# Optimization experiments

Hardware: AMD Instinct MI355X
Metric: run time of the kernel (lower is better)

The kernel has to match this reference:

```python
import jax, jax.numpy as jnp
import numpy as np

B, D_IN, NF = 8192, 64, 128
D1 = 1 + D_IN              # 65  : first linear input (bias col + x)
O1 = 1 + NF                # 129 : o width after first layer
IN2 = O1 + NF * NF         # 16513 : polylayer-1 input width
O2 = O1 + NF               # 257
IN3 = O2 + NF * NF         # 16641 : polylayer-2 input width
FC_IN = 1 + 3 * NF + 3 * NF  # 769 : cat(o, og) width


def setup_inputs() -> dict:
    key = jax.random.key(0)
    ks = jax.random.split(key, 16)
    w = lambda k, shape: jax.random.normal(k, shape, jnp.float32) * 0.02
    return {
        "x": jax.random.normal(ks[0], (B, D_IN), jnp.float32),
        "bias0": jnp.asarray(1.0, jnp.float32),
        "Wf1": w(ks[1], (D1, NF)), "bf1": w(ks[2], (NF,)),
        "Wg1": w(ks[3], (D1, NF)), "bg1": w(ks[4], (NF,)),
        "Wf2": w(ks[5], (IN2, NF)), "bf2": w(ks[6], (NF,)),
        "Wg2": w(ks[7], (IN2, NF)), "bg2": w(ks[8], (NF,)),
        "Wf3": w(ks[9], (IN3, NF)), "bf3": w(ks[10], (NF,)),
        "Wg3": w(ks[11], (IN3, NF)), "bg3": w(ks[12], (NF,)),
        "Wfc": w(ks[13], (FC_IN, 1)), "bfc": w(ks[14], (1,)),
    }


def reference(x, bias0, Wf1, bf1, Wg1, bg1, Wf2, bf2, Wg2, bg2,
              Wf3, bf3, Wg3, bg3, Wfc, bfc):
    Bn = x.shape[0]
    o = jnp.ones((Bn, 1), x.dtype) * bias0          # bias column
    z = jnp.concatenate([o, x], axis=1)              # [B, 1+D_in]
    og = z @ Wg1 + bg1                               # vanishing branch
    ot = z @ Wf1 + bf1                               # nonvanishing branch
    o1 = ot                                          # degree-1 features, kept fixed
    o = jnp.concatenate([o, ot], axis=1)
    for Wf, bf, Wg, bg in ((Wf2, bf2, Wg2, bg2), (Wf3, bf3, Wg3, bg3)):
        # batched outer product o1_i ot_i^T, row-major flatten -> [B, nf1*nf_t]
        outer = (o1[:, :, None] * ot[:, None, :]).reshape(Bn, -1)
        xx = jnp.concatenate([o, outer], axis=1)
        xf = xx @ Wf + bf
        xg = xx @ Wg + bg
        ot = xf
        o = jnp.concatenate([o, xf], axis=1)
        og = jnp.concatenate([og, xg], axis=1)
    return jnp.concatenate([o, og], axis=1) @ Wfc + bfc
```

## Files before the change

kernel.cpp:

```cpp
#include <hip/hip_runtime.h>

typedef _Float16 f16;
typedef _Float16 f16x8 __attribute__((ext_vector_type(8)));
typedef float f32x4 __attribute__((ext_vector_type(4)));

static constexpr size_t PART_STRIDE = (size_t)8192 * 256;

static constexpr size_t OFF_W2   = 0;
static constexpr size_t SZ_W2    = (size_t)516 * 8192 * 2;
static constexpr size_t OFF_W3   = OFF_W2 + SZ_W2;
static constexpr size_t SZ_W3    = (size_t)520 * 8192 * 2;
static constexpr size_t OFF_OT1  = OFF_W3 + SZ_W3;
static constexpr size_t OFF_XF2  = OFF_OT1 + (size_t)8192 * 128 * 2;
static constexpr size_t OFF_C2   = OFF_XF2 + (size_t)8192 * 128 * 2;
static constexpr size_t OFF_C3   = OFF_C2 + 1024;
static constexpr size_t OFF_ACC  = OFF_C3 + 1024;
static constexpr size_t OFF_PART = OFF_ACC + 32768;

template<int LAYER>
__global__ __launch_bounds__(256)
void prep_w(const float* __restrict__ Wf, const float* __restrict__ Wg,
            f16* __restrict__ Wswz)
{
    const int t = blockIdx.x * 256 + threadIdx.x;
    const int s = t >> 10, rem = t & 1023;
    const int nt = rem >> 6, l = rem & 63;
    const int n = nt * 16 + (l & 15);
    const int klb = (l >> 4) * 8;
    f16x8 o;
#pragma unroll
    for (int e = 0; e < 8; ++e) {
        const int kl = klb + e;
        int row;
        if (LAYER == 2) {
            if (s < 4) row = 1 + s * 32 + kl;
            else { const int u = s - 4; row = 129 + (u & 127) * 128 + (u >> 7) * 32 + kl; }
        } else {
            if (s < 8) row = 1 + s * 32 + kl;
            else { const int u = s - 8; row = 257 + (u & 127) * 128 + (u >> 7) * 32 + kl; }
        }
        const float v = (n < 128) ? Wf[(size_t)row * 128 + n]
                                  : Wg[(size_t)row * 128 + (n - 128)];
        o[e] = (f16)v;
    }
    *(f16x8*)(Wswz + (size_t)t * 8) = o;
}

__global__ __launch_bounds__(256)
void prep_small(const float* __restrict__ bias0,
                const float* __restrict__ Wf2, const float* __restrict__ bf2,
                const float* __restrict__ Wg2, const float* __restrict__ bg2,
                const float* __restrict__ Wf3, const float* __restrict__ bf3,
                const float* __restrict__ Wg3, const float* __restrict__ bg3,
                float* __restrict__ c2, float* __restrict__ c3)
{
    const int n = threadIdx.x;
    const float b0 = bias0[0];
    if (n < 128) { c2[n] = bf2[n] + b0 * Wf2[n]; c3[n] = bf3[n] + b0 * Wf3[n]; }
    else { const int m = n - 128; c2[n] = bg2[m] + b0 * Wg2[m]; c3[n] = bg3[m] + b0 * Wg3[m]; }
}

__global__ __launch_bounds__(256)
void layer1_poly(const float* __restrict__ x, const float* __restrict__ bias0,
                 const float* __restrict__ Wf1, const float* __restrict__ bf1,
                 const float* __restrict__ Wg1, const float* __restrict__ bg1,
                 const float* __restrict__ Wfc, const float* __restrict__ bfc,
                 f16* __restrict__ ot1f16, float* __restrict__ outacc)
{
    const int half = threadIdx.x >> 7;
    const int n = threadIdx.x & 127;
    const int r = blockIdx.x * 2 + half;
    const float b0 = bias0[0];
    float sf = b0 * Wf1[n] + bf1[n];
    float sg = b0 * Wg1[n] + bg1[n];
    const float* xr = x + (size_t)r * 64;
#pragma unroll 8
    for (int k = 0; k < 64; ++k) {
        const float xv = xr[k];
        sf = fmaf(xv, Wf1[(k + 1) * 128 + n], sf);
        sg = fmaf(xv, Wg1[(k + 1) * 128 + n], sg);
    }
    ot1f16[(size_t)r * 128 + n] = (f16)sf;
    float p = sf * Wfc[1 + n] + sg * Wfc[385 + n];
#pragma unroll
    for (int off = 32; off; off >>= 1) p += __shfl_down(p, off);
    __shared__ float wp[4];
    if ((threadIdx.x & 63) == 0) wp[threadIdx.x >> 6] = p;
    __syncthreads();
    if ((threadIdx.x & 127) == 0)
        outacc[r] = bfc[0] + b0 * Wfc[0] + wp[half * 2] + wp[half * 2 + 1];
}


#define STAGE(S_W, BUF) do {                                                        \
    const f16* _src = wsrc0 + (size_t)(S_W) * 8192;                                 \
    __builtin_amdgcn_global_load_lds(                                               \
        (const __attribute__((address_space(1))) unsigned int*)_src,                \
        (__attribute__((address_space(3))) unsigned int*)&wbuf[BUF][tid * 8],       \
        16, 0, 0);                                                                  \
} while (0)

#define GBODY(O1CUR, O1NXT, I8)                                                     \
{                                                                                   \
    _Pragma("unroll")                                                               \
    for (int e = 0; e < 8; ++e) {                                                   \
        const int cc = (I8) * 8 + e;                                                \
        if (e < 7) { STAGE(out_base + cc + 1, (CLIN + e + 1) & 1); }                \
        else if ((I8) < 15) { STAGE(out_base + cc + 1, (CLIN + e + 1) & 1); }       \
        if (e == 0) {                                                               \
            _Pragma("unroll")                                                       \
            for (int mi = 0; mi < 8; ++mi)                                          \
                O1NXT[mi] = *(const f16x8*)(ot1_row + mi * 2048 + ((I8) + 1) * 8);  \
        }                                                                           \
        f16x8 afr[8];                                                               \
        _Pragma("unroll")                                                           \
        for (int mi = 0; mi < 8; ++mi)                                              \
            afr[mi] = featreg[mi] * O1CUR[mi][e];                                   \
        const f16* wb = &wbuf[(CLIN + e) & 1][0];                                   \
        _Pragma("unroll")                                                           \
        for (int ni = 0; ni < 2; ++ni) {                                            \
            const f16x8 bfr = *(const f16x8*)(wb + ((wc * 2 + ni) * 64 + lane) * 8);\
            _Pragma("unroll")                                                       \
            for (int mi = 0; mi < 8; ++mi)                                          \
                acc[mi][ni] = __builtin_amdgcn_mfma_f32_16x16x32_f16(               \
                    afr[mi], bfr, acc[mi][ni], 0, 0, 0);                            \
        }                                                                           \
        __syncthreads();                                                            \
    }                                                                               \
}

template<int LAYER>
__global__ __launch_bounds__(256, 2)
void gemm_poly(const f16* __restrict__ Wswz, const f16* featg,
               const f16* ot1g, float* __restrict__ partials)
{
    __shared__ f16 wbuf[2][2048];

    constexpr int NLIN = (LAYER == 2) ? 4 : 8;
    constexpr int CLIN = (LAYER == 2) ? 1 : 2;

    const int bid = blockIdx.x;
    const int rb = bid >> 4;
    const int sp = (bid >> 2) & 3;
    const int nb = bid & 3;
    const int r0 = rb * 256;
    const int tid = threadIdx.x;
    const int wid = tid >> 6, lane = tid & 63;
    const int wr = wid >> 1, wc = wid & 1;
    const int lhi = lane >> 4, llo = lane & 15;

    const f16* wsrc0 = Wswz + nb * 2048 + tid * 8;
    const f16* ot1_row  = ot1g  + (size_t)(r0 + wr * 128 + llo) * 128;
    const f16* feat_row = featg + (size_t)(r0 + wr * 128 + llo) * 128;

    f32x4 acc[8][2] = {};
    const int out_base = NLIN + sp * 128;

    STAGE(CLIN * sp, 0);
    f16x8 featreg[8], o1A[8], o1B[8];
#pragma unroll
    for (int mi = 0; mi < 8; ++mi) {
        featreg[mi] = *(const f16x8*)(feat_row + mi * 2048 + sp * 32 + lhi * 8);
        o1A[mi]     = *(const f16x8*)(ot1_row + mi * 2048);
    }
    __syncthreads();

#pragma unroll
    for (int c = 0; c < CLIN; ++c) {
        const int s = CLIN * sp + c;
        STAGE((c + 1 < CLIN) ? (s + 1) : out_base, (c + 1) & 1);
        f16x8 afr[8];
        const int col = s * 32 + lhi * 8;
#pragma unroll
        for (int mi = 0; mi < 8; ++mi) {
            if (LAYER == 2) afr[mi] = *(const f16x8*)(ot1_row + mi * 2048 + col);
            else afr[mi] = (col < 128) ? *(const f16x8*)(ot1_row + mi * 2048 + col)
                                       : *(const f16x8*)(feat_row + mi * 2048 + (col - 128));
        }
        const f16* wb = &wbuf[c & 1][0];
#pragma unroll
        for (int ni = 0; ni < 2; ++ni) {
            const f16x8 bfr = *(const f16x8*)(wb + ((wc * 2 + ni) * 64 + lane) * 8);
#pragma unroll
            for (int mi = 0; mi < 8; ++mi)
                acc[mi][ni] = __builtin_amdgcn_mfma_f32_16x16x32_f16(afr[mi], bfr, acc[mi][ni], 0, 0, 0);
        }
        __syncthreads();
    }

    for (int i8 = 0; i8 < 16; i8 += 2) {
        GBODY(o1A, o1B, i8);
        GBODY(o1B, o1A, i8 + 1);
    }

    float* pout = partials + (size_t)sp * PART_STRIDE
                + (size_t)(r0 + wr * 128) * 256 + nb * 64 + wc * 32 + llo;
#pragma unroll
    for (int mi = 0; mi < 8; ++mi)
#pragma unroll
        for (int ni = 0; ni < 2; ++ni)
#pragma unroll
            for (int q = 0; q < 4; ++q)
                pout[(size_t)(mi * 16 + lhi * 4 + q) * 256 + ni * 16] = acc[mi][ni][q];
}

#undef GBODY
#undef STAGE

template<int LAYER>
__global__ __launch_bounds__(256)
void reduce_poly(const float* __restrict__ partials, const float* __restrict__ cvec,
                 const float* __restrict__ Wfc, f16* __restrict__ xf_out,
                 float* __restrict__ outacc, float* __restrict__ outp)
{
    const int r = blockIdx.x;
    const int n = threadIdx.x;
    const size_t idx = (size_t)r * 256 + n;
    float v = partials[idx] + partials[idx + PART_STRIDE]
            + partials[idx + 2 * PART_STRIDE] + partials[idx + 3 * PART_STRIDE];
    v += cvec[n];
    if (LAYER == 2 && n < 128)
        xf_out[(size_t)r * 128 + n] = (f16)v;
    const int wseg = (LAYER == 2) ? (n < 128 ? 129 + n : 513 + (n - 128))
                                  : (n < 128 ? 257 + n : 641 + (n - 128));
    float p = v * Wfc[wseg];
#pragma unroll
    for (int off = 32; off; off >>= 1) p += __shfl_down(p, off);
    __shared__ float wp[4];
    if ((threadIdx.x & 63) == 0) wp[threadIdx.x >> 6] = p;
    __syncthreads();
    if (threadIdx.x == 0) {
        const float tot = wp[0] + wp[1] + wp[2] + wp[3];
        if (LAYER == 2) outacc[r] += tot;
        else            outp[r] = outacc[r] + tot;
    }
}

extern "C" void kernel_launch(void* const* d_in, const int* in_sizes, int n_in,
                              void* d_out, int out_size, void* d_ws, size_t ws_size,
                              hipStream_t stream)
{
    (void)in_sizes; (void)n_in; (void)out_size; (void)ws_size;
    const float* x     = (const float*)d_in[0];
    const float* bias0 = (const float*)d_in[1];
    const float* Wf1   = (const float*)d_in[2];
    const float* bf1   = (const float*)d_in[3];
    const float* Wg1   = (const float*)d_in[4];
    const float* bg1   = (const float*)d_in[5];
    const float* Wf2   = (const float*)d_in[6];
    const float* bf2   = (const float*)d_in[7];
    const float* Wg2   = (const float*)d_in[8];
    const float* bg2   = (const float*)d_in[9];
    const float* Wf3   = (const float*)d_in[10];
    const float* bf3   = (const float*)d_in[11];
    const float* Wg3   = (const float*)d_in[12];
    const float* bg3   = (const float*)d_in[13];
    const float* Wfc   = (const float*)d_in[14];
    const float* bfc   = (const float*)d_in[15];
    float* out = (float*)d_out;

    char* ws = (char*)d_ws;
    f16*   W2s    = (f16*)(ws + OFF_W2);
    f16*   W3s    = (f16*)(ws + OFF_W3);
    f16*   ot1f16 = (f16*)(ws + OFF_OT1);
    f16*   xf2f16 = (f16*)(ws + OFF_XF2);
    float* c2     = (float*)(ws + OFF_C2);
    float* c3     = (float*)(ws + OFF_C3);
    float* outacc = (float*)(ws + OFF_ACC);
    float* parts  = (float*)(ws + OFF_PART);

    prep_w<2><<<2064, 256, 0, stream>>>(Wf2, Wg2, W2s);
    prep_w<3><<<2080, 256, 0, stream>>>(Wf3, Wg3, W3s);
    prep_small<<<1, 256, 0, stream>>>(bias0, Wf2, bf2, Wg2, bg2, Wf3, bf3, Wg3, bg3, c2, c3);
    layer1_poly<<<4096, 256, 0, stream>>>(x, bias0, Wf1, bf1, Wg1, bg1, Wfc, bfc, ot1f16, outacc);
    gemm_poly<2><<<512, 256, 0, stream>>>(W2s, ot1f16, ot1f16, parts);
    reduce_poly<2><<<8192, 256, 0, stream>>>(parts, c2, Wfc, xf2f16, outacc, out);
    gemm_poly<3><<<512, 256, 0, stream>>>(W3s, xf2f16, ot1f16, parts);
    reduce_poly<3><<<8192, 256, 0, stream>>>(parts, c3, Wfc, nullptr, outacc, out);
}
```

Before: 312.6 us.

## Load B fragments straight from global into registers, drop LDS staging and barriers

The poly GEMM no longer stages weight tiles through double-buffered LDS with a barrier per k-step. Each wave now loads its own B fragment directly from global memory into registers, using a two-deep register prefetch. The N tile per block is halved (one 16-column fragment per wave), the grid doubles to 1024 blocks, and launch bounds allow 4 blocks per CU. This removes synchronisation and LDS traffic and raises occupancy. In exchange, each wave issues global loads with less latency hiding, the A fragment products are recomputed for half as many columns, and more blocks redundantly load the same A rows.

```diff
diff --git a/kernel.cpp b/kernel.cpp
--- a/kernel.cpp
+++ b/kernel.cpp
@@ -92,120 +92,92 @@
 }
 
 
-#define STAGE(S_W, BUF) do {                                                        \
-    const f16* _src = wsrc0 + (size_t)(S_W) * 8192;                                 \
-    __builtin_amdgcn_global_load_lds(                                               \
-        (const __attribute__((address_space(1))) unsigned int*)_src,                \
-        (__attribute__((address_space(3))) unsigned int*)&wbuf[BUF][tid * 8],       \
-        16, 0, 0);                                                                  \
-} while (0)
-
-#define GBODY(O1CUR, O1NXT, I8)                                                     \
+#define OBODY(O1CUR, O1NXT, I8)                                                     \
 {                                                                                   \
     _Pragma("unroll")                                                               \
     for (int e = 0; e < 8; ++e) {                                                   \
         const int cc = (I8) * 8 + e;                                                \
-        if (e < 7) { STAGE(out_base + cc + 1, (CLIN + e + 1) & 1); }                \
-        else if ((I8) < 15) { STAGE(out_base + cc + 1, (CLIN + e + 1) & 1); }       \
+        f16x8 bC = {};                                                              \
+        if (cc + 2 < 128)                                                           \
+            bC = *(const f16x8*)(wB + (size_t)(out_base + cc + 2) * 8192);          \
         if (e == 0) {                                                               \
             _Pragma("unroll")                                                       \
             for (int mi = 0; mi < 8; ++mi)                                          \
                 O1NXT[mi] = *(const f16x8*)(ot1_row + mi * 2048 + ((I8) + 1) * 8);  \
         }                                                                           \
-        f16x8 afr[8];                                                               \
         _Pragma("unroll")                                                           \
-        for (int mi = 0; mi < 8; ++mi)                                              \
-            afr[mi] = featreg[mi] * O1CUR[mi][e];                                   \
-        const f16* wb = &wbuf[(CLIN + e) & 1][0];                                   \
-        _Pragma("unroll")                                                           \
-        for (int ni = 0; ni < 2; ++ni) {                                            \
-            const f16x8 bfr = *(const f16x8*)(wb + ((wc * 2 + ni) * 64 + lane) * 8);\
-            _Pragma("unroll")                                                       \
-            for (int mi = 0; mi < 8; ++mi)                                          \
-                acc[mi][ni] = __builtin_amdgcn_mfma_f32_16x16x32_f16(               \
-                    afr[mi], bfr, acc[mi][ni], 0, 0, 0);                            \
+        for (int mi = 0; mi < 8; ++mi) {                                            \
+            const f16x8 a = featreg[mi] * O1CUR[mi][e];                             \
+            acc[mi] = __builtin_amdgcn_mfma_f32_16x16x32_f16(a, bA, acc[mi], 0, 0, 0);\
         }                                                                           \
-        __syncthreads();                                                            \
+        bA = bB; bB = bC;                                                           \
     }                                                                               \
 }
 
 template<int LAYER>
-__global__ __launch_bounds__(256, 2)
+__global__ __launch_bounds__(256, 4)
 void gemm_poly(const f16* __restrict__ Wswz, const f16* featg,
                const f16* ot1g, float* __restrict__ partials)
 {
-    __shared__ f16 wbuf[2][2048];
-
     constexpr int NLIN = (LAYER == 2) ? 4 : 8;
     constexpr int CLIN = (LAYER == 2) ? 1 : 2;
 
     const int bid = blockIdx.x;
-    const int rb = bid >> 4;
-    const int sp = (bid >> 2) & 3;
-    const int nb = bid & 3;
+    const int rb = bid >> 5;
+    const int sp = (bid >> 3) & 3;
+    const int nb = bid & 7;
     const int r0 = rb * 256;
     const int tid = threadIdx.x;
     const int wid = tid >> 6, lane = tid & 63;
     const int wr = wid >> 1, wc = wid & 1;
     const int lhi = lane >> 4, llo = lane & 15;
 
-    const f16* wsrc0 = Wswz + nb * 2048 + tid * 8;
+    const f16* wB = Wswz + nb * 1024 + wc * 512 + lane * 8;
     const f16* ot1_row  = ot1g  + (size_t)(r0 + wr * 128 + llo) * 128;
     const f16* feat_row = featg + (size_t)(r0 + wr * 128 + llo) * 128;
 
-    f32x4 acc[8][2] = {};
+    f32x4 acc[8] = {};
     const int out_base = NLIN + sp * 128;
 
-    STAGE(CLIN * sp, 0);
     f16x8 featreg[8], o1A[8], o1B[8];
 #pragma unroll
     for (int mi = 0; mi < 8; ++mi) {
         featreg[mi] = *(const f16x8*)(feat_row + mi * 2048 + sp * 32 + lhi * 8);
         o1A[mi]     = *(const f16x8*)(ot1_row + mi * 2048);
     }
-    __syncthreads();
+    f16x8 bA = *(const f16x8*)(wB + (size_t)(out_base + 0) * 8192);
+    f16x8 bB = *(const f16x8*)(wB + (size_t)(out_base + 1) * 8192);
 
 #pragma unroll
     for (int c = 0; c < CLIN; ++c) {
         const int s = CLIN * sp + c;
-        STAGE((c + 1 < CLIN) ? (s + 1) : out_base, (c + 1) & 1);
-        f16x8 afr[8];
+        const f16x8 b = *(const f16x8*)(wB + (size_t)s * 8192);
         const int col = s * 32 + lhi * 8;
 #pragma unroll
         for (int mi = 0; mi < 8; ++mi) {
-            if (LAYER == 2) afr[mi] = *(const f16x8*)(ot1_row + mi * 2048 + col);
-            else afr[mi] = (col < 128) ? *(const f16x8*)(ot1_row + mi * 2048 + col)
-                                       : *(const f16x8*)(feat_row + mi * 2048 + (col - 128));
+            f16x8 a;
+            if (LAYER == 2) a = *(const f16x8*)(ot1_row + mi * 2048 + col);
+            else a = (col < 128) ? *(const f16x8*)(ot1_row + mi * 2048 + col)
+                                 : *(const f16x8*)(feat_row + mi * 2048 + (col - 128));
+            acc[mi] = __builtin_amdgcn_mfma_f32_16x16x32_f16(a, b, acc[mi], 0, 0, 0);
         }
-        const f16* wb = &wbuf[c & 1][0];
-#pragma unroll
-        for (int ni = 0; ni < 2; ++ni) {
-            const f16x8 bfr = *(const f16x8*)(wb + ((wc * 2 + ni) * 64 + lane) * 8);
-#pragma unroll
-            for (int mi = 0; mi < 8; ++mi)
-                acc[mi][ni] = __builtin_amdgcn_mfma_f32_16x16x32_f16(afr[mi], bfr, acc[mi][ni], 0, 0, 0);
-        }
-        __syncthreads();
     }
 
     for (int i8 = 0; i8 < 16; i8 += 2) {
-        GBODY(o1A, o1B, i8);
-        GBODY(o1B, o1A, i8 + 1);
+        OBODY(o1A, o1B, i8);
+        OBODY(o1B, o1A, i8 + 1);
     }
 
     float* pout = partials + (size_t)sp * PART_STRIDE
-                + (size_t)(r0 + wr * 128) * 256 + nb * 64 + wc * 32 + llo;
+                + (size_t)(r0 + wr * 128) * 256 + nb * 32 + wc * 16 + llo;
 #pragma unroll
     for (int mi = 0; mi < 8; ++mi)
 #pragma unroll
-        for (int ni = 0; ni < 2; ++ni)
-#pragma unroll
-            for (int q = 0; q < 4; ++q)
-                pout[(size_t)(mi * 16 + lhi * 4 + q) * 256 + ni * 16] = acc[mi][ni][q];
-}
-
-#undef GBODY
-#undef STAGE
+        for (int q = 0; q < 4; ++q)
+            pout[(size_t)(mi * 16 + lhi * 4 + q) * 256] = acc[mi][q];
+}
+
+#undef OBODY
 
 template<int LAYER>
 __global__ __launch_bounds__(256)
@@ -273,8 +245,8 @@
     prep_w<3><<<2080, 256, 0, stream>>>(Wf3, Wg3, W3s);
     prep_small<<<1, 256, 0, stream>>>(bias0, Wf2, bf2, Wg2, bg2, Wf3, bf3, Wg3, bg3, c2, c3);
     layer1_poly<<<4096, 256, 0, stream>>>(x, bias0, Wf1, bf1, Wg1, bg1, Wfc, bfc, ot1f16, outacc);
-    gemm_poly<2><<<512, 256, 0, stream>>>(W2s, ot1f16, ot1f16, parts);
+    gemm_poly<2><<<1024, 256, 0, stream>>>(W2s, ot1f16, ot1f16, parts);
     reduce_poly<2><<<8192, 256, 0, stream>>>(parts, c2, Wfc, xf2f16, outacc, out);
-    gemm_poly<3><<<512, 256, 0, stream>>>(W3s, xf2f16, ot1f16, parts);
+    gemm_poly<3><<<1024, 256, 0, stream>>>(W3s, xf2f16, ot1f16, parts);
     reduce_poly<3><<<8192, 256, 0, stream>>>(parts, c3, Wfc, nullptr, outacc, out);
 }
```

Measured after the change: 368.1 us. 1.18x slower.

## Fuse prep kernels into one launch and triple-buffer weight staging in GEMM

Applied to the files above, without the earlier changes.

Merges the two weight-swizzle kernels, the bias-constant kernel and the layer-1 kernel into a single launch that dispatches work by block index, removing three launch gaps. In the GEMM, the double-buffered LDS weight staging with a full __syncthreads per step becomes a 3-deep ring. Each step uses an explicit vmcnt wait plus s_barrier, so the async global-to-LDS load of step s+2 overlaps the MFMAs of step s. This adds LDS use and depends on the hand-written waitcnt counts being correct. It also issues a redundant tail stage load.

```diff
diff --git a/kernel.cpp b/kernel.cpp
--- a/kernel.cpp
+++ b/kernel.cpp
@@ -18,11 +18,10 @@
 static constexpr size_t OFF_PART = OFF_ACC + 32768;
 
 template<int LAYER>
-__global__ __launch_bounds__(256)
-void prep_w(const float* __restrict__ Wf, const float* __restrict__ Wg,
-            f16* __restrict__ Wswz)
-{
-    const int t = blockIdx.x * 256 + threadIdx.x;
+__device__ __forceinline__
+void prep_w_body(int t, const float* __restrict__ Wf, const float* __restrict__ Wg,
+                 f16* __restrict__ Wswz)
+{
     const int s = t >> 10, rem = t & 1023;
     const int nt = rem >> 6, l = rem & 63;
     const int n = nt * 16 + (l & 15);
@@ -47,48 +46,52 @@
 }
 
 __global__ __launch_bounds__(256)
-void prep_small(const float* __restrict__ bias0,
+void prep_fused(const float* __restrict__ x, const float* __restrict__ bias0,
+                const float* __restrict__ Wf1, const float* __restrict__ bf1,
+                const float* __restrict__ Wg1, const float* __restrict__ bg1,
                 const float* __restrict__ Wf2, const float* __restrict__ bf2,
                 const float* __restrict__ Wg2, const float* __restrict__ bg2,
                 const float* __restrict__ Wf3, const float* __restrict__ bf3,
                 const float* __restrict__ Wg3, const float* __restrict__ bg3,
-                float* __restrict__ c2, float* __restrict__ c3)
-{
-    const int n = threadIdx.x;
-    const float b0 = bias0[0];
-    if (n < 128) { c2[n] = bf2[n] + b0 * Wf2[n]; c3[n] = bf3[n] + b0 * Wf3[n]; }
-    else { const int m = n - 128; c2[n] = bg2[m] + b0 * Wg2[m]; c3[n] = bg3[m] + b0 * Wg3[m]; }
-}
-
-__global__ __launch_bounds__(256)
-void layer1_poly(const float* __restrict__ x, const float* __restrict__ bias0,
-                 const float* __restrict__ Wf1, const float* __restrict__ bf1,
-                 const float* __restrict__ Wg1, const float* __restrict__ bg1,
-                 const float* __restrict__ Wfc, const float* __restrict__ bfc,
-                 f16* __restrict__ ot1f16, float* __restrict__ outacc)
-{
-    const int half = threadIdx.x >> 7;
-    const int n = threadIdx.x & 127;
-    const int r = blockIdx.x * 2 + half;
-    const float b0 = bias0[0];
-    float sf = b0 * Wf1[n] + bf1[n];
-    float sg = b0 * Wg1[n] + bg1[n];
-    const float* xr = x + (size_t)r * 64;
+                const float* __restrict__ Wfc, const float* __restrict__ bfc,
+                f16* __restrict__ W2s, f16* __restrict__ W3s,
+                float* __restrict__ c2, float* __restrict__ c3,
+                f16* __restrict__ ot1f16, float* __restrict__ outacc)
+{
+    const int bid = blockIdx.x;
+    __shared__ float wp[4];
+    if (bid < 2064) {
+        prep_w_body<2>(bid * 256 + threadIdx.x, Wf2, Wg2, W2s);
+    } else if (bid < 4144) {
+        prep_w_body<3>((bid - 2064) * 256 + threadIdx.x, Wf3, Wg3, W3s);
+    } else if (bid == 4144) {
+        const int n = threadIdx.x;
+        const float b0 = bias0[0];
+        if (n < 128) { c2[n] = bf2[n] + b0 * Wf2[n]; c3[n] = bf3[n] + b0 * Wf3[n]; }
+        else { const int m = n - 128; c2[n] = bg2[m] + b0 * Wg2[m]; c3[n] = bg3[m] + b0 * Wg3[m]; }
+    } else {
+        const int half = threadIdx.x >> 7;
+        const int n = threadIdx.x & 127;
+        const int r = (bid - 4145) * 2 + half;
+        const float b0 = bias0[0];
+        float sf = b0 * Wf1[n] + bf1[n];
+        float sg = b0 * Wg1[n] + bg1[n];
+        const float* xr = x + (size_t)r * 64;
 #pragma unroll 8
-    for (int k = 0; k < 64; ++k) {
-        const float xv = xr[k];
-        sf = fmaf(xv, Wf1[(k + 1) * 128 + n], sf);
-        sg = fmaf(xv, Wg1[(k + 1) * 128 + n], sg);
-    }
-    ot1f16[(size_t)r * 128 + n] = (f16)sf;
-    float p = sf * Wfc[1 + n] + sg * Wfc[385 + n];
-#pragma unroll
-    for (int off = 32; off; off >>= 1) p += __shfl_down(p, off);
-    __shared__ float wp[4];
-    if ((threadIdx.x & 63) == 0) wp[threadIdx.x >> 6] = p;
-    __syncthreads();
-    if ((threadIdx.x & 127) == 0)
-        outacc[r] = bfc[0] + b0 * Wfc[0] + wp[half * 2] + wp[half * 2 + 1];
+        for (int k = 0; k < 64; ++k) {
+            const float xv = xr[k];
+            sf = fmaf(xv, Wf1[(k + 1) * 128 + n], sf);
+            sg = fmaf(xv, Wg1[(k + 1) * 128 + n], sg);
+        }
+        ot1f16[(size_t)r * 128 + n] = (f16)sf;
+        float p = sf * Wfc[1 + n] + sg * Wfc[385 + n];
+#pragma unroll
+        for (int off = 32; off; off >>= 1) p += __shfl_down(p, off);
+        if ((threadIdx.x & 63) == 0) wp[threadIdx.x >> 6] = p;
+        __syncthreads();
+        if ((threadIdx.x & 127) == 0)
+            outacc[r] = bfc[0] + b0 * Wfc[0] + wp[half * 2] + wp[half * 2 + 1];
+    }
 }
 
 
@@ -96,45 +99,55 @@
     const f16* _src = wsrc0 + (size_t)(S_W) * 8192;                                 \
     __builtin_amdgcn_global_load_lds(                                               \
         (const __attribute__((address_space(1))) unsigned int*)_src,                \
-        (__attribute__((address_space(3))) unsigned int*)&wbuf[BUF][tid * 8],       \
+        (__attribute__((address_space(3))) unsigned int*)&wring[BUF][tid * 8],      \
         16, 0, 0);                                                                  \
 } while (0)
 
-#define GBODY(O1CUR, O1NXT, I8)                                                     \
+#define WAITVX(N) asm volatile("s_waitcnt vmcnt(" #N ") lgkmcnt(0)" ::: "memory")
+#define WAITV(N) WAITVX(N)
+
+#define RSTEP(O1CUR, O1NXT, I8, E, WN, LN)                                          \
 {                                                                                   \
-    _Pragma("unroll")                                                               \
-    for (int e = 0; e < 8; ++e) {                                                   \
-        const int cc = (I8) * 8 + e;                                                \
-        if (e < 7) { STAGE(out_base + cc + 1, (CLIN + e + 1) & 1); }                \
-        else if ((I8) < 15) { STAGE(out_base + cc + 1, (CLIN + e + 1) & 1); }       \
-        if (e == 0) {                                                               \
-            _Pragma("unroll")                                                       \
-            for (int mi = 0; mi < 8; ++mi)                                          \
-                O1NXT[mi] = *(const f16x8*)(ot1_row + mi * 2048 + ((I8) + 1) * 8);  \
-        }                                                                           \
-        f16x8 afr[8];                                                               \
+    const int s_ = (I8) * 8 + (E);                                                  \
+    WAITV(WN);                                                                      \
+    __builtin_amdgcn_s_barrier();                                                   \
+    __builtin_amdgcn_sched_barrier(0);                                              \
+    {                                                                               \
+        const int sn_ = (s_ + 2 < 128) ? s_ + 2 : 127;           \
+        STAGE(out_base + sn_, (s_ + 2) % 3);                                        \
+    }                                                                               \
+    if ((LN) && (E) == 0) {                                                         \
         _Pragma("unroll")                                                           \
         for (int mi = 0; mi < 8; ++mi)                                              \
-            afr[mi] = featreg[mi] * O1CUR[mi][e];                                   \
-        const f16* wb = &wbuf[(CLIN + e) & 1][0];                                   \
-        _Pragma("unroll")                                                           \
-        for (int ni = 0; ni < 2; ++ni) {                                            \
-            const f16x8 bfr = *(const f16x8*)(wb + ((wc * 2 + ni) * 64 + lane) * 8);\
-            _Pragma("unroll")                                                       \
-            for (int mi = 0; mi < 8; ++mi)                                          \
-                acc[mi][ni] = __builtin_amdgcn_mfma_f32_16x16x32_f16(               \
-                    afr[mi], bfr, acc[mi][ni], 0, 0, 0);                            \
-        }                                                                           \
-        __syncthreads();                                                            \
+            O1NXT[mi] = *(const f16x8*)(ot1_row + mi * 2048 + ((I8) + 1) * 8);      \
     }                                                                               \
-}
+    const f16* wb_ = &wring[s_ % 3][0];                                             \
+    const f16x8 b0_ = *(const f16x8*)(wb_ + (wc * 128 + lane) * 8);                 \
+    const f16x8 b1_ = *(const f16x8*)(wb_ + (wc * 128 + 64 + lane) * 8);            \
+    _Pragma("unroll")                                                               \
+    for (int mi = 0; mi < 8; ++mi) {                                                \
+        const f16x8 a_ = featreg[mi] * O1CUR[mi][E];                                \
+        acc[mi][0] = __builtin_amdgcn_mfma_f32_16x16x32_f16(a_, b0_, acc[mi][0], 0, 0, 0); \
+        acc[mi][1] = __builtin_amdgcn_mfma_f32_16x16x32_f16(a_, b1_, acc[mi][1], 0, 0, 0); \
+    }                                                                               \
+}
+
+#define RBODY(O1CUR, O1NXT, I8, W1, LN)     \
+    RSTEP(O1CUR, O1NXT, I8, 0, 1, LN)       \
+    RSTEP(O1CUR, O1NXT, I8, 1, W1, LN)      \
+    RSTEP(O1CUR, O1NXT, I8, 2, 1, LN)       \
+    RSTEP(O1CUR, O1NXT, I8, 3, 1, LN)       \
+    RSTEP(O1CUR, O1NXT, I8, 4, 1, LN)       \
+    RSTEP(O1CUR, O1NXT, I8, 5, 1, LN)       \
+    RSTEP(O1CUR, O1NXT, I8, 6, 1, LN)       \
+    RSTEP(O1CUR, O1NXT, I8, 7, 1, LN)
 
 template<int LAYER>
 __global__ __launch_bounds__(256, 2)
 void gemm_poly(const f16* __restrict__ Wswz, const f16* featg,
                const f16* ot1g, float* __restrict__ partials)
 {
-    __shared__ f16 wbuf[2][2048];
+    __shared__ f16 wring[3][2048];
 
     constexpr int NLIN = (LAYER == 2) ? 4 : 8;
     constexpr int CLIN = (LAYER == 2) ? 1 : 2;
@@ -156,42 +169,44 @@
     f32x4 acc[8][2] = {};
     const int out_base = NLIN + sp * 128;
 
-    STAGE(CLIN * sp, 0);
     f16x8 featreg[8], o1A[8], o1B[8];
 #pragma unroll
     for (int mi = 0; mi < 8; ++mi) {
         featreg[mi] = *(const f16x8*)(feat_row + mi * 2048 + sp * 32 + lhi * 8);
         o1A[mi]     = *(const f16x8*)(ot1_row + mi * 2048);
     }
+
+    STAGE(CLIN * sp, 0);
     __syncthreads();
-
 #pragma unroll
     for (int c = 0; c < CLIN; ++c) {
+        if (c + 1 < CLIN) STAGE(CLIN * sp + c + 1, 1);
         const int s = CLIN * sp + c;
-        STAGE((c + 1 < CLIN) ? (s + 1) : out_base, (c + 1) & 1);
-        f16x8 afr[8];
         const int col = s * 32 + lhi * 8;
+        const f16* wb = &wring[c][0];
+        const f16x8 b0 = *(const f16x8*)(wb + (wc * 128 + lane) * 8);
+        const f16x8 b1 = *(const f16x8*)(wb + (wc * 128 + 64 + lane) * 8);
 #pragma unroll
         for (int mi = 0; mi < 8; ++mi) {
-            if (LAYER == 2) afr[mi] = *(const f16x8*)(ot1_row + mi * 2048 + col);
-            else afr[mi] = (col < 128) ? *(const f16x8*)(ot1_row + mi * 2048 + col)
-                                       : *(const f16x8*)(feat_row + mi * 2048 + (col - 128));
-        }
-        const f16* wb = &wbuf[c & 1][0];
-#pragma unroll
-        for (int ni = 0; ni < 2; ++ni) {
-            const f16x8 bfr = *(const f16x8*)(wb + ((wc * 2 + ni) * 64 + lane) * 8);
-#pragma unroll
-            for (int mi = 0; mi < 8; ++mi)
-                acc[mi][ni] = __builtin_amdgcn_mfma_f32_16x16x32_f16(afr[mi], bfr, acc[mi][ni], 0, 0, 0);
+            f16x8 a;
+            if (LAYER == 2) a = *(const f16x8*)(ot1_row + mi * 2048 + col);
+            else a = (col < 128) ? *(const f16x8*)(ot1_row + mi * 2048 + col)
+                                 : *(const f16x8*)(feat_row + mi * 2048 + (col - 128));
+            acc[mi][0] = __builtin_amdgcn_mfma_f32_16x16x32_f16(a, b0, acc[mi][0], 0, 0, 0);
+            acc[mi][1] = __builtin_amdgcn_mfma_f32_16x16x32_f16(a, b1, acc[mi][1], 0, 0, 0);
         }
         __syncthreads();
     }
 
-    for (int i8 = 0; i8 < 16; i8 += 2) {
-        GBODY(o1A, o1B, i8);
-        GBODY(o1B, o1A, i8 + 1);
-    }
+    STAGE(out_base + 0, 0);
+    STAGE(out_base + 1, 1);
+
+    for (int i8 = 0; i8 < 14; i8 += 2) {
+        RBODY(o1A, o1B, i8,     9, 1)
+        RBODY(o1B, o1A, i8 + 1, 9, 1)
+    }
+    RBODY(o1A, o1B, 14, 9, 1)
+    RBODY(o1B, o1A, 15, 1, 0)
 
     float* pout = partials + (size_t)sp * PART_STRIDE
                 + (size_t)(r0 + wr * 128) * 256 + nb * 64 + wc * 32 + llo;
@@ -204,7 +219,10 @@
                 pout[(size_t)(mi * 16 + lhi * 4 + q) * 256 + ni * 16] = acc[mi][ni][q];
 }
 
-#undef GBODY
+#undef RBODY
+#undef RSTEP
+#undef WAITV
+#undef WAITVX
 #undef STAGE
 
 template<int LAYER>
@@ -269,10 +287,9 @@
     float* outacc = (float*)(ws + OFF_ACC);
     float* parts  = (float*)(ws + OFF_PART);
 
-    prep_w<2><<<2064, 256, 0, stream>>>(Wf2, Wg2, W2s);
-    prep_w<3><<<2080, 256, 0, stream>>>(Wf3, Wg3, W3s);
-    prep_small<<<1, 256, 0, stream>>>(bias0, Wf2, bf2, Wg2, bg2, Wf3, bf3, Wg3, bg3, c2, c3);
-    layer1_poly<<<4096, 256, 0, stream>>>(x, bias0, Wf1, bf1, Wg1, bg1, Wfc, bfc, ot1f16, outacc);
+    prep_fused<<<8241, 256, 0, stream>>>(x, bias0, Wf1, bf1, Wg1, bg1,
+                                         Wf2, bf2, Wg2, bg2, Wf3, bf3, Wg3, bg3,
+                                         Wfc, bfc, W2s, W3s, c2, c3, ot1f16, outacc);
     gemm_poly<2><<<512, 256, 0, stream>>>(W2s, ot1f16, ot1f16, parts);
     reduce_poly<2><<<8192, 256, 0, stream>>>(parts, c2, Wfc, xf2f16, outacc, out);
     gemm_poly<3><<<512, 256, 0, stream>>>(W3s, xf2f16, ot1f16, parts);
```

New measurement: 295.9 us. 1.06x faster.
